# Performance work log

Measured on AMD Instinct MI355X. Metric: run time of the kernel, lower is better.

## Reference

```python
import jax, jax.numpy as jnp
import numpy as np

NUM_GROUPS = 5
EPS = 1e-5
QB = 128.0  # 2**(8-1) for b=8 activation quantization


def _binarize_weights_groupwise(W):
    """Sign-binarize W group-wise along out-feature dim, STE on backward.
    Faithful to torch: rows beyond num_groups*group_size remain zero."""
    n_out = W.shape[0]
    gs = n_out // NUM_GROUPS
    Wb = jnp.zeros_like(W)
    for g in range(NUM_GROUPS):  # small fixed loop (5 groups)
        wg = W[g * gs:(g + 1) * gs]
        z = wg - wg.mean()
        # STE: forward = sign(z), backward = identity w.r.t. z
        ste = z + jax.lax.stop_gradient(jnp.sign(z) - z)
        Wb = Wb.at[g * gs:(g + 1) * gs].set(ste)
    return Wb


def _quantize_activations_groupwise(x):
    """8-bit absmax quantization group-wise along dim 0 (batch), per torch code."""
    n = x.shape[0]
    gs = n // NUM_GROUPS
    xq = jnp.zeros_like(x)
    for g in range(NUM_GROUPS):
        ag = x[g * gs:(g + 1) * gs]
        gamma = jnp.max(jnp.abs(ag))
        xq = xq.at[g * gs:(g + 1) * gs].set(
            jnp.clip(ag * QB / (gamma + EPS), -QB + EPS, QB - EPS))
    return xq


def _bitlinear(x, W, b):
    Wb = _binarize_weights_groupwise(W)
    y = jnp.einsum('btc,oc->bto', x, Wb) + b
    return _quantize_activations_groupwise(y)


def setup_inputs() -> dict:
    key = jax.random.key(0)
    k1, k2, k3, k4, k5 = jax.random.split(key, 5)
    B, T, C = 10, 2048, 384
    H = 4 * C
    lim1 = 1.0 / np.sqrt(C)
    lim2 = 1.0 / np.sqrt(H)
    x = jax.random.normal(k1, (B, T, C), dtype=jnp.float32)
    W1 = jax.random.uniform(k2, (H, C), minval=-lim1, maxval=lim1, dtype=jnp.float32)
    b1 = jax.random.uniform(k3, (H,), minval=-lim1, maxval=lim1, dtype=jnp.float32)
    W2 = jax.random.uniform(k4, (C, H), minval=-lim2, maxval=lim2, dtype=jnp.float32)
    b2 = jax.random.uniform(k5, (C,), minval=-lim2, maxval=lim2, dtype=jnp.float32)
    return {"x": x, "W1": W1, "b1": b1, "W2": W2, "b2": b2}


def reference(x, W1, b1, W2, b2):
    h = _bitlinear(x, W1, b1)           # [B,T,4C], quantized to [-128,128]
    h = jax.nn.gelu(h, approximate=False)  # torch nn.GELU default is exact
    out = _bitlinear(h, W2, b2)         # [B,T,C]
    return out  # nn.Dropout is identity in eval/reference mode
```

## Files before the change

### kernel.cpp

```cpp
#include <hip/hip_runtime.h>
#include <cstdint>
#include <cstddef>

#define THREADS 256
#define NB 8

typedef float f32x4 __attribute__((ext_vector_type(4)));
typedef __bf16 bf16x8 __attribute__((ext_vector_type(8)));
typedef __bf16 bf16x4 __attribute__((ext_vector_type(4)));

__device__ __forceinline__ void gload_lds16(const void* g, void* l) {
    auto gp = (const __attribute__((address_space(1))) unsigned int*)(unsigned long long)(uintptr_t)g;
    auto lp = (__attribute__((address_space(3))) unsigned int*)(unsigned int)(uintptr_t)l;
    __builtin_amdgcn_global_load_lds(gp, lp, 16, 0, 0);
}

__global__ void zero_gamma(unsigned int* p) {
    if (threadIdx.x < 16) p[threadIdx.x] = 0u;
}

__global__ void group_partial_sums(const float* __restrict__ W, float* __restrict__ partials,
                                   int elems_per_group) {
    const int g = blockIdx.y, b = blockIdx.x;
    const int tid = threadIdx.x;
    const int chunk4 = elems_per_group / (4 * NB);
    const float* base = W + (size_t)g * elems_per_group + (size_t)b * chunk4 * 4;
    float s = 0.f;
    for (int i = tid; i < chunk4; i += THREADS) {
        f32x4 v = *reinterpret_cast<const f32x4*>(base + 4 * (size_t)i);
        s += (v[0] + v[1]) + (v[2] + v[3]);
    }
    __shared__ float red[THREADS];
    red[tid] = s;
    __syncthreads();
    for (int off = THREADS / 2; off > 0; off >>= 1) {
        if (tid < off) red[tid] += red[tid + off];
        __syncthreads();
    }
    if (tid == 0) partials[g * NB + b] = red[0];
}

__global__ void binarize_apply(const float* __restrict__ W, __bf16* __restrict__ Wb,
                               const float* __restrict__ partials,
                               int elems_per_group, int tail_elems) {
    const int g = blockIdx.y, b = blockIdx.x;
    const int tid = threadIdx.x;
    if (g == 5) {
        if (b != 0) return;
        __bf16* og = Wb + (size_t)5 * elems_per_group;
        for (int i = tid; i < tail_elems; i += THREADS) og[i] = (__bf16)0.f;
        return;
    }
    float total = 0.f;
#pragma unroll
    for (int j = 0; j < NB; ++j) total += partials[g * NB + j];
    const float mean = total / (float)elems_per_group;

    const int chunk4 = elems_per_group / (4 * NB);
    const size_t off0 = (size_t)g * elems_per_group + (size_t)b * chunk4 * 4;
    const float* base = W + off0;
    __bf16* ob = Wb + off0;
    for (int i = tid; i < chunk4; i += THREADS) {
        f32x4 v = *reinterpret_cast<const f32x4*>(base + 4 * (size_t)i);
        bf16x4 o;
#pragma unroll
        for (int j = 0; j < 4; ++j) {
            const float z = v[j] - mean;
            o[j] = (__bf16)((z > 0.f) ? 1.f : ((z < 0.f) ? -1.f : 0.f));
        }
        *reinterpret_cast<bf16x4*>(ob + 4 * (size_t)i) = o;
    }
}

__global__ __launch_bounds__(512, 2)
void gemm1_f32a(const float* __restrict__ A, const __bf16* __restrict__ Bw,
                const float* __restrict__ bias, __bf16* __restrict__ outp,
                unsigned int* __restrict__ gmax, int M, int N, int K,
                int GN, int nwg) {
    constexpr int BM = 256, BN = 256, BK = 64, NF = 4;
    constexpr int ABYTES = BM * BK * 2;
    constexpr int BBYTES = BN * BK * 2;
    __shared__ __attribute__((aligned(16))) char lds[2 * (ABYTES + BBYTES)];

    const int tid = threadIdx.x;
    const int wave = tid >> 6, lane = tid & 63;
    const int l15 = lane & 15, l4 = lane >> 4;
    const int wr = wave >> 2, wc = wave & 3;

    const int cpx = nwg >> 3;
    const int orig = (blockIdx.x & 7) * cpx + (blockIdx.x >> 3);
    const int bm = orig / GN, bn = orig % GN;

    const int arow = tid >> 1;
    const int ach = tid & 1;
    const float* Aptr = A + (size_t)(bm * BM + arow) * K + ach * 32;
    const __bf16* Bb = Bw + (size_t)bn * BN * K;
    const int NT = K / BK;

    f32x4 acc[8][NF];
#pragma unroll
    for (int m = 0; m < 8; ++m)
#pragma unroll
        for (int n = 0; n < NF; ++n)
            acc[m][n] = f32x4{0.f, 0.f, 0.f, 0.f};

    f32x4 areg[8];
    auto LOADA = [&](int t) {
        const float* p = Aptr + t * BK;
#pragma unroll
        for (int j = 0; j < 8; ++j)
            areg[j] = *reinterpret_cast<const f32x4*>(p + j * 4);
    };
    auto WRITEA = [&](int t) {
        char* ab = lds + (t & 1) * (ABYTES + BBYTES);
#pragma unroll
        for (int j = 0; j < 4; ++j) {
            bf16x8 w;
#pragma unroll
            for (int e = 0; e < 4; ++e) {
                w[e]     = (__bf16)areg[2 * j][e];
                w[e + 4] = (__bf16)areg[2 * j + 1][e];
            }
            const int s = ach * 4 + j;
            *reinterpret_cast<bf16x8*>(
                ab + arow * 128 + ((s ^ (arow & 7)) << 4)) = w;
        }
    };
    auto STAGEB = [&](int t) {
        char* bb = lds + (t & 1) * (ABYTES + BBYTES) + ABYTES;
#pragma unroll
        for (int j = 0; j < 4; ++j) {
            const int q = j * 8192 + tid * 16;
            const int lr = q >> 7;
            const int s = ((q >> 4) & 7) ^ (lr & 7);
            gload_lds16(Bb + (size_t)lr * K + t * BK + s * 8, bb + q);
        }
    };

    LOADA(0); STAGEB(0);
    asm volatile("s_waitcnt vmcnt(0)" ::: "memory");
    WRITEA(0);
    __syncthreads();

    for (int t = 0; t < NT; ++t) {
        if (t + 1 < NT) { LOADA(t + 1); STAGEB(t + 1); }
        const char* ab = lds + (t & 1) * (ABYTES + BBYTES);
        const char* bb = ab + ABYTES;
#pragma unroll
        for (int kk = 0; kk < 2; ++kk) {
            bf16x8 af[8], bfv[NF];
#pragma unroll
            for (int m = 0; m < 8; ++m) {
                const int r = wr * 128 + m * 16 + l15;
                const int sp = (kk * 4 + l4) ^ (r & 7);
                af[m] = *reinterpret_cast<const bf16x8*>(ab + r * 128 + sp * 16);
            }
#pragma unroll
            for (int n = 0; n < NF; ++n) {
                const int r = wc * 64 + n * 16 + l15;
                const int sp = (kk * 4 + l4) ^ (r & 7);
                bfv[n] = *reinterpret_cast<const bf16x8*>(bb + r * 128 + sp * 16);
            }
#pragma unroll
            for (int m = 0; m < 8; ++m)
#pragma unroll
                for (int n = 0; n < NF; ++n)
                    acc[m][n] = __builtin_amdgcn_mfma_f32_16x16x32_bf16(
                        bfv[n], af[m], acc[m][n], 0, 0, 0);
        }
        if (t + 1 < NT) {
            asm volatile("s_waitcnt vmcnt(0)" ::: "memory");
            WRITEA(t + 1);
        }
        __syncthreads();
    }

    const int rowb = bm * BM + wr * 128;
    const int colb = bn * BN + wc * 64;
    float lmax = 0.f;
#pragma unroll
    for (int n = 0; n < NF; ++n) {
        const f32x4 bv = *reinterpret_cast<const f32x4*>(bias + colb + n * 16 + l4 * 4);
#pragma unroll
        for (int m = 0; m < 8; ++m) {
            const int row = rowb + m * 16 + l15;
            bf16x4 o;
#pragma unroll
            for (int r = 0; r < 4; ++r) {
                const float v = acc[m][n][r] + bv[r];
                lmax = fmaxf(lmax, fabsf(v));
                o[r] = (__bf16)v;
            }
            *reinterpret_cast<bf16x4*>(
                &outp[(size_t)row * N + colb + n * 16 + l4 * 4]) = o;
        }
    }
#pragma unroll
    for (int off = 32; off > 0; off >>= 1)
        lmax = fmaxf(lmax, __shfl_down(lmax, off, 64));
    float* wredmax = (float*)lds;
    if (lane == 0) wredmax[wave] = lmax;
    __syncthreads();
    if (tid == 0) {
        float bmax = wredmax[0];
#pragma unroll
        for (int w = 1; w < 8; ++w) bmax = fmaxf(bmax, wredmax[w]);
        atomicMax(gmax + (bm * BM) / 4096, __float_as_uint(bmax));
    }
}

__global__ __launch_bounds__(512, 2)
void gemm2_bt(const __bf16* __restrict__ A, const __bf16* __restrict__ Bw,
              const float* __restrict__ bias, float* __restrict__ outp,
              unsigned int* __restrict__ gmax, int M, int N, int K,
              int GN, int nwg) {
    constexpr int BM = 256, BN_ = 128, BK = 64, NF = 2;
    constexpr int ABYTES = BM * BK * 2;
    constexpr int BBYTES = BN_ * BK * 2;
    __shared__ __attribute__((aligned(16))) char lds[2 * (ABYTES + BBYTES)];

    const int tid = threadIdx.x;
    const int wave = tid >> 6, lane = tid & 63;
    const int l15 = lane & 15, l4 = lane >> 4;
    const int wr = wave >> 2, wc = wave & 3;

    const int cpx = nwg >> 3;
    const int orig = (blockIdx.x & 7) * cpx + (blockIdx.x >> 3);
    const int bm = orig / GN, bn = orig % GN;

    const __bf16* Ab = A + (size_t)bm * BM * K;
    const __bf16* Bb = Bw + (size_t)bn * BN_ * K;
    const int NT = K / BK;

    f32x4 acc[8][NF];
#pragma unroll
    for (int m = 0; m < 8; ++m)
#pragma unroll
        for (int n = 0; n < NF; ++n)
            acc[m][n] = f32x4{0.f, 0.f, 0.f, 0.f};

    auto STAGE = [&](int t) {
        const int k0 = t * BK;
        char* ab = lds + (t & 1) * (ABYTES + BBYTES);
        char* bb = ab + ABYTES;
#pragma unroll
        for (int j = 0; j < 4; ++j) {
            const int q = j * 8192 + tid * 16;
            const int lr = q >> 7;
            const int s = ((q >> 4) & 7) ^ (lr & 7);
            gload_lds16(Ab + (size_t)lr * K + k0 + s * 8, ab + q);
        }
#pragma unroll
        for (int j = 0; j < 2; ++j) {
            const int q = j * 8192 + tid * 16;
            const int lr = q >> 7;
            const int s = ((q >> 4) & 7) ^ (lr & 7);
            gload_lds16(Bb + (size_t)lr * K + k0 + s * 8, bb + q);
        }
    };

    STAGE(0);
    asm volatile("s_waitcnt vmcnt(0)" ::: "memory");
    __syncthreads();

    for (int t = 0; t < NT; ++t) {
        if (t + 1 < NT) STAGE(t + 1);
        const char* ab = lds + (t & 1) * (ABYTES + BBYTES);
        const char* bb = ab + ABYTES;
#pragma unroll
        for (int kk = 0; kk < 2; ++kk) {
            bf16x8 af[8], bfv[NF];
#pragma unroll
            for (int m = 0; m < 8; ++m) {
                const int r = wr * 128 + m * 16 + l15;
                const int sp = (kk * 4 + l4) ^ (r & 7);
                af[m] = *reinterpret_cast<const bf16x8*>(ab + r * 128 + sp * 16);
            }
#pragma unroll
            for (int n = 0; n < NF; ++n) {
                const int r = wc * 32 + n * 16 + l15;
                const int sp = (kk * 4 + l4) ^ (r & 7);
                bfv[n] = *reinterpret_cast<const bf16x8*>(bb + r * 128 + sp * 16);
            }
#pragma unroll
            for (int m = 0; m < 8; ++m)
#pragma unroll
                for (int n = 0; n < NF; ++n)
                    acc[m][n] = __builtin_amdgcn_mfma_f32_16x16x32_bf16(
                        bfv[n], af[m], acc[m][n], 0, 0, 0);
        }
        asm volatile("s_waitcnt vmcnt(0)" ::: "memory");
        __syncthreads();
    }

    const int rowb = bm * BM + wr * 128;
    const int colb = bn * BN_ + wc * 32;
    float lmax = 0.f;
#pragma unroll
    for (int n = 0; n < NF; ++n) {
        const f32x4 bv = *reinterpret_cast<const f32x4*>(bias + colb + n * 16 + l4 * 4);
#pragma unroll
        for (int m = 0; m < 8; ++m) {
            const int row = rowb + m * 16 + l15;
            f32x4 o;
#pragma unroll
            for (int r = 0; r < 4; ++r) {
                o[r] = acc[m][n][r] + bv[r];
                lmax = fmaxf(lmax, fabsf(o[r]));
            }
            *reinterpret_cast<f32x4*>(
                &outp[(size_t)row * N + colb + n * 16 + l4 * 4]) = o;
        }
    }
#pragma unroll
    for (int off = 32; off > 0; off >>= 1)
        lmax = fmaxf(lmax, __shfl_down(lmax, off, 64));
    float* wredmax = (float*)lds;
    if (lane == 0) wredmax[wave] = lmax;
    __syncthreads();
    if (tid == 0) {
        float bmax = wredmax[0];
#pragma unroll
        for (int w = 1; w < 8; ++w) bmax = fmaxf(bmax, wredmax[w]);
        atomicMax(gmax + (bm * BM) / 4096, __float_as_uint(bmax));
    }
}

__global__ void quant_gelu(__bf16* __restrict__ y, const unsigned int* __restrict__ gbits,
                           int perg8, int n8) {
    int i = blockIdx.x * blockDim.x + threadIdx.x;
    if (i >= n8) return;
    const int g = i / perg8;
    const float gamma = __uint_as_float(gbits[g]);
    const float s = 128.0f / (gamma + 1e-5f);
    bf16x8 v = *reinterpret_cast<const bf16x8*>(y + 8 * (size_t)i);
    bf16x8 o;
#pragma unroll
    for (int j = 0; j < 8; ++j) {
        float f = (float)v[j] * s;
        f = fminf(fmaxf(f, -128.0f + 1e-5f), 128.0f - 1e-5f);
        const float ge = 0.5f * f * (1.0f + erff(f * 0.70710678118654752f));
        o[j] = (__bf16)ge;
    }
    *reinterpret_cast<bf16x8*>(y + 8 * (size_t)i) = o;
}

__global__ void final_scale(float* __restrict__ y, const unsigned int* __restrict__ gbits,
                            int perg4, int n4) {
    int i = blockIdx.x * blockDim.x + threadIdx.x;
    if (i >= n4) return;
    const int g = i / perg4;
    const float gamma = __uint_as_float(gbits[g]);
    const float s = 128.0f / (gamma + 1e-5f);
    f32x4 v = *reinterpret_cast<const f32x4*>(y + 4 * (size_t)i);
    f32x4 o;
#pragma unroll
    for (int j = 0; j < 4; ++j)
        o[j] = fminf(fmaxf(v[j] * s, -128.0f + 1e-5f), 128.0f - 1e-5f);
    *reinterpret_cast<f32x4*>(y + 4 * (size_t)i) = o;
}

extern "C" void kernel_launch(void* const* d_in, const int* in_sizes, int n_in,
                              void* d_out, int out_size, void* d_ws, size_t ws_size,
                              hipStream_t stream) {
    const float* x  = (const float*)d_in[0];
    const float* W1 = (const float*)d_in[1];
    const float* b1 = (const float*)d_in[2];
    const float* W2 = (const float*)d_in[3];
    const float* b2 = (const float*)d_in[4];
    float* out = (float*)d_out;

    const int BB = 10, TT = 2048, C = 384, H = 1536;
    const int M = BB * TT;

    const int gs1 = H / 5;
    const int gs2 = C / 5;
    const int epg1 = gs1 * C;
    const int epg2 = gs2 * H;
    const int tail1 = (H - 5 * gs1) * C;
    const int tail2 = (C - 5 * gs2) * H;

    const size_t szW1b = (size_t)H * C * 2;
    const size_t szW2b = (size_t)C * H * 2;
    const size_t szY1  = (size_t)M * H * 2;

    char* p = (char*)d_ws;
    __bf16* W1b = (__bf16*)p; p += szW1b;
    __bf16* W2b = (__bf16*)p; p += szW2b;
    __bf16* y1  = (__bf16*)p; p += szY1;
    unsigned int* gamma = (unsigned int*)p; p += 64;
    float* psums = (float*)p; p += 2 * 5 * NB * 4;
    if ((size_t)(p - (char*)d_ws) > ws_size) return;

    zero_gamma<<<1, 64, 0, stream>>>(gamma);

    group_partial_sums<<<dim3(NB, 5), THREADS, 0, stream>>>(W1, psums, epg1);
    group_partial_sums<<<dim3(NB, 5), THREADS, 0, stream>>>(W2, psums + 5 * NB, epg2);
    binarize_apply<<<dim3(NB, 6), THREADS, 0, stream>>>(W1, W1b, psums, epg1, tail1);
    binarize_apply<<<dim3(NB, 6), THREADS, 0, stream>>>(W2, W2b, psums + 5 * NB, epg2, tail2);

    gemm1_f32a<<<480, 512, 0, stream>>>(
        x, W1b, b1, y1, gamma, M, H, C, H / 256, 480);

    quant_gelu<<<(M * H / 8 + THREADS - 1) / THREADS, THREADS, 0, stream>>>(
        y1, gamma, (M / 5) * H / 8, M * H / 8);

    gemm2_bt<<<240, 512, 0, stream>>>(
        y1, W2b, b2, out, gamma + 5, M, C, H, C / 128, 240);

    final_scale<<<(M * C / 4 + THREADS - 1) / THREADS, THREADS, 0, stream>>>(
        out, gamma + 5, (M / 5) * C / 4, M * C / 4);
}
```

Before: 162.9 us.

## Fuse quantize+GELU into GEMM2 A-load and pre-convert x to bf16

The standalone quant_gelu pass over the M×H intermediate is removed. GEMM2 now loads raw bf16 GEMM1 output into registers, applies group scale, clamp and exact GELU, and writes the result to LDS. In exchange, GEMM1 takes a bf16 copy of x made by a new conversion kernel, so it can use direct global-to-LDS loads for both operands. This saves a full read-write pass of the large intermediate, but each GEMM2 tile recomputes erf for its A tile three times (once per N block) and adds an extra kernel plus an x copy.

```diff
diff --git a/kernel.cpp b/kernel.cpp
--- a/kernel.cpp
+++ b/kernel.cpp
@@ -72,14 +72,23 @@
     }
 }
 
+__global__ void cvt_f32_bf16(const float* __restrict__ in, __bf16* __restrict__ ot, int n4) {
+    int i = blockIdx.x * blockDim.x + threadIdx.x;
+    if (i >= n4) return;
+    f32x4 v = *reinterpret_cast<const f32x4*>(in + 4 * (size_t)i);
+    bf16x4 o;
+    o[0] = (__bf16)v[0]; o[1] = (__bf16)v[1]; o[2] = (__bf16)v[2]; o[3] = (__bf16)v[3];
+    *reinterpret_cast<bf16x4*>(ot + 4 * (size_t)i) = o;
+}
+
 __global__ __launch_bounds__(512, 2)
-void gemm1_f32a(const float* __restrict__ A, const __bf16* __restrict__ Bw,
-                const float* __restrict__ bias, __bf16* __restrict__ outp,
-                unsigned int* __restrict__ gmax, int M, int N, int K,
-                int GN, int nwg) {
-    constexpr int BM = 256, BN = 256, BK = 64, NF = 4;
+void gemm1_bt(const __bf16* __restrict__ A, const __bf16* __restrict__ Bw,
+              const float* __restrict__ bias, __bf16* __restrict__ outp,
+              unsigned int* __restrict__ gmax, int M, int N, int K,
+              int GN, int nwg) {
+    constexpr int BM = 256, BN_ = 256, BK = 64, NF = 4;
     constexpr int ABYTES = BM * BK * 2;
-    constexpr int BBYTES = BN * BK * 2;
+    constexpr int BBYTES = BN_ * BK * 2;
     __shared__ __attribute__((aligned(16))) char lds[2 * (ABYTES + BBYTES)];
 
     const int tid = threadIdx.x;
@@ -91,10 +100,8 @@
     const int orig = (blockIdx.x & 7) * cpx + (blockIdx.x >> 3);
     const int bm = orig / GN, bn = orig % GN;
 
-    const int arow = tid >> 1;
-    const int ach = tid & 1;
-    const float* Aptr = A + (size_t)(bm * BM + arow) * K + ach * 32;
-    const __bf16* Bb = Bw + (size_t)bn * BN * K;
+    const __bf16* Ab = A + (size_t)bm * BM * K;
+    const __bf16* Bb = Bw + (size_t)bn * BN_ * K;
     const int NT = K / BK;
 
     f32x4 acc[8][NF];
@@ -104,46 +111,32 @@
         for (int n = 0; n < NF; ++n)
             acc[m][n] = f32x4{0.f, 0.f, 0.f, 0.f};
 
-    f32x4 areg[8];
-    auto LOADA = [&](int t) {
-        const float* p = Aptr + t * BK;
-#pragma unroll
-        for (int j = 0; j < 8; ++j)
-            areg[j] = *reinterpret_cast<const f32x4*>(p + j * 4);
-    };
-    auto WRITEA = [&](int t) {
+    auto STAGE = [&](int t) {
+        const int k0 = t * BK;
         char* ab = lds + (t & 1) * (ABYTES + BBYTES);
-#pragma unroll
-        for (int j = 0; j < 4; ++j) {
-            bf16x8 w;
-#pragma unroll
-            for (int e = 0; e < 4; ++e) {
-                w[e]     = (__bf16)areg[2 * j][e];
-                w[e + 4] = (__bf16)areg[2 * j + 1][e];
-            }
-            const int s = ach * 4 + j;
-            *reinterpret_cast<bf16x8*>(
-                ab + arow * 128 + ((s ^ (arow & 7)) << 4)) = w;
-        }
-    };
-    auto STAGEB = [&](int t) {
-        char* bb = lds + (t & 1) * (ABYTES + BBYTES) + ABYTES;
+        char* bb = ab + ABYTES;
 #pragma unroll
         for (int j = 0; j < 4; ++j) {
             const int q = j * 8192 + tid * 16;
             const int lr = q >> 7;
             const int s = ((q >> 4) & 7) ^ (lr & 7);
-            gload_lds16(Bb + (size_t)lr * K + t * BK + s * 8, bb + q);
+            gload_lds16(Ab + (size_t)lr * K + k0 + s * 8, ab + q);
+        }
+#pragma unroll
+        for (int j = 0; j < 4; ++j) {
+            const int q = j * 8192 + tid * 16;
+            const int lr = q >> 7;
+            const int s = ((q >> 4) & 7) ^ (lr & 7);
+            gload_lds16(Bb + (size_t)lr * K + k0 + s * 8, bb + q);
         }
     };
 
-    LOADA(0); STAGEB(0);
+    STAGE(0);
     asm volatile("s_waitcnt vmcnt(0)" ::: "memory");
-    WRITEA(0);
     __syncthreads();
 
     for (int t = 0; t < NT; ++t) {
-        if (t + 1 < NT) { LOADA(t + 1); STAGEB(t + 1); }
+        if (t + 1 < NT) STAGE(t + 1);
         const char* ab = lds + (t & 1) * (ABYTES + BBYTES);
         const char* bb = ab + ABYTES;
 #pragma unroll
@@ -168,15 +161,12 @@
                     acc[m][n] = __builtin_amdgcn_mfma_f32_16x16x32_bf16(
                         bfv[n], af[m], acc[m][n], 0, 0, 0);
         }
-        if (t + 1 < NT) {
-            asm volatile("s_waitcnt vmcnt(0)" ::: "memory");
-            WRITEA(t + 1);
-        }
+        asm volatile("s_waitcnt vmcnt(0)" ::: "memory");
         __syncthreads();
     }
 
     const int rowb = bm * BM + wr * 128;
-    const int colb = bn * BN + wc * 64;
+    const int colb = bn * BN_ + wc * 64;
     float lmax = 0.f;
 #pragma unroll
     for (int n = 0; n < NF; ++n) {
@@ -210,10 +200,11 @@
 }
 
 __global__ __launch_bounds__(512, 2)
-void gemm2_bt(const __bf16* __restrict__ A, const __bf16* __restrict__ Bw,
-              const float* __restrict__ bias, float* __restrict__ outp,
-              unsigned int* __restrict__ gmax, int M, int N, int K,
-              int GN, int nwg) {
+void gemm2_fused(const __bf16* __restrict__ A, const __bf16* __restrict__ Bw,
+                 const float* __restrict__ bias, float* __restrict__ outp,
+                 const unsigned int* __restrict__ g1bits,
+                 unsigned int* __restrict__ gmax, int M, int N, int K,
+                 int GN, int nwg) {
     constexpr int BM = 256, BN_ = 128, BK = 64, NF = 2;
     constexpr int ABYTES = BM * BK * 2;
     constexpr int BBYTES = BN_ * BK * 2;
@@ -228,7 +219,11 @@
     const int orig = (blockIdx.x & 7) * cpx + (blockIdx.x >> 3);
     const int bm = orig / GN, bn = orig % GN;
 
-    const __bf16* Ab = A + (size_t)bm * BM * K;
+    const float s1 = 128.0f / (__uint_as_float(g1bits[bm >> 4]) + 1e-5f);
+
+    const int arow = tid >> 1;
+    const int ach = tid & 1;
+    const __bf16* Aptr = A + (size_t)(bm * BM + arow) * K + ach * 32;
     const __bf16* Bb = Bw + (size_t)bn * BN_ * K;
     const int NT = K / BK;
 
@@ -239,32 +234,47 @@
         for (int n = 0; n < NF; ++n)
             acc[m][n] = f32x4{0.f, 0.f, 0.f, 0.f};
 
-    auto STAGE = [&](int t) {
-        const int k0 = t * BK;
+    bf16x8 areg[4];
+    auto LOADA = [&](int t) {
+        const __bf16* p = Aptr + t * BK;
+#pragma unroll
+        for (int j = 0; j < 4; ++j)
+            areg[j] = *reinterpret_cast<const bf16x8*>(p + j * 8);
+    };
+    auto GELU_WRITEA = [&](int t) {
         char* ab = lds + (t & 1) * (ABYTES + BBYTES);
-        char* bb = ab + ABYTES;
 #pragma unroll
         for (int j = 0; j < 4; ++j) {
-            const int q = j * 8192 + tid * 16;
-            const int lr = q >> 7;
-            const int s = ((q >> 4) & 7) ^ (lr & 7);
-            gload_lds16(Ab + (size_t)lr * K + k0 + s * 8, ab + q);
-        }
+            bf16x8 w;
+#pragma unroll
+            for (int e = 0; e < 8; ++e) {
+                float f = (float)areg[j][e] * s1;
+                f = fminf(fmaxf(f, -128.0f + 1e-5f), 128.0f - 1e-5f);
+                w[e] = (__bf16)(0.5f * f * (1.0f + erff(f * 0.70710678118654752f)));
+            }
+            const int s = ach * 4 + j;
+            *reinterpret_cast<bf16x8*>(
+                ab + arow * 128 + ((s ^ (arow & 7)) << 4)) = w;
+        }
+    };
+    auto STAGEB = [&](int t) {
+        char* bb = lds + (t & 1) * (ABYTES + BBYTES) + ABYTES;
 #pragma unroll
         for (int j = 0; j < 2; ++j) {
             const int q = j * 8192 + tid * 16;
             const int lr = q >> 7;
             const int s = ((q >> 4) & 7) ^ (lr & 7);
-            gload_lds16(Bb + (size_t)lr * K + k0 + s * 8, bb + q);
+            gload_lds16(Bb + (size_t)lr * K + t * BK + s * 8, bb + q);
         }
     };
 
-    STAGE(0);
+    LOADA(0); STAGEB(0);
     asm volatile("s_waitcnt vmcnt(0)" ::: "memory");
+    GELU_WRITEA(0);
     __syncthreads();
 
     for (int t = 0; t < NT; ++t) {
-        if (t + 1 < NT) STAGE(t + 1);
+        if (t + 1 < NT) { LOADA(t + 1); STAGEB(t + 1); }
         const char* ab = lds + (t & 1) * (ABYTES + BBYTES);
         const char* bb = ab + ABYTES;
 #pragma unroll
@@ -290,6 +300,7 @@
                         bfv[n], af[m], acc[m][n], 0, 0, 0);
         }
         asm volatile("s_waitcnt vmcnt(0)" ::: "memory");
+        if (t + 1 < NT) GELU_WRITEA(t + 1);
         __syncthreads();
     }
 
@@ -324,25 +335,6 @@
         for (int w = 1; w < 8; ++w) bmax = fmaxf(bmax, wredmax[w]);
         atomicMax(gmax + (bm * BM) / 4096, __float_as_uint(bmax));
     }
-}
-
-__global__ void quant_gelu(__bf16* __restrict__ y, const unsigned int* __restrict__ gbits,
-                           int perg8, int n8) {
-    int i = blockIdx.x * blockDim.x + threadIdx.x;
-    if (i >= n8) return;
-    const int g = i / perg8;
-    const float gamma = __uint_as_float(gbits[g]);
-    const float s = 128.0f / (gamma + 1e-5f);
-    bf16x8 v = *reinterpret_cast<const bf16x8*>(y + 8 * (size_t)i);
-    bf16x8 o;
-#pragma unroll
-    for (int j = 0; j < 8; ++j) {
-        float f = (float)v[j] * s;
-        f = fminf(fmaxf(f, -128.0f + 1e-5f), 128.0f - 1e-5f);
-        const float ge = 0.5f * f * (1.0f + erff(f * 0.70710678118654752f));
-        o[j] = (__bf16)ge;
-    }
-    *reinterpret_cast<bf16x8*>(y + 8 * (size_t)i) = o;
 }
 
 __global__ void final_scale(float* __restrict__ y, const unsigned int* __restrict__ gbits,
@@ -382,11 +374,13 @@
 
     const size_t szW1b = (size_t)H * C * 2;
     const size_t szW2b = (size_t)C * H * 2;
+    const size_t szXb  = (size_t)M * C * 2;
     const size_t szY1  = (size_t)M * H * 2;
 
     char* p = (char*)d_ws;
     __bf16* W1b = (__bf16*)p; p += szW1b;
     __bf16* W2b = (__bf16*)p; p += szW2b;
+    __bf16* xb  = (__bf16*)p; p += szXb;
     __bf16* y1  = (__bf16*)p; p += szY1;
     unsigned int* gamma = (unsigned int*)p; p += 64;
     float* psums = (float*)p; p += 2 * 5 * NB * 4;
@@ -399,14 +393,13 @@
     binarize_apply<<<dim3(NB, 6), THREADS, 0, stream>>>(W1, W1b, psums, epg1, tail1);
     binarize_apply<<<dim3(NB, 6), THREADS, 0, stream>>>(W2, W2b, psums + 5 * NB, epg2, tail2);
 
-    gemm1_f32a<<<480, 512, 0, stream>>>(
-        x, W1b, b1, y1, gamma, M, H, C, H / 256, 480);
-
-    quant_gelu<<<(M * H / 8 + THREADS - 1) / THREADS, THREADS, 0, stream>>>(
-        y1, gamma, (M / 5) * H / 8, M * H / 8);
-
-    gemm2_bt<<<240, 512, 0, stream>>>(
-        y1, W2b, b2, out, gamma + 5, M, C, H, C / 128, 240);
+    cvt_f32_bf16<<<(M * C / 4 + THREADS - 1) / THREADS, THREADS, 0, stream>>>(x, xb, M * C / 4);
+
+    gemm1_bt<<<480, 512, 0, stream>>>(
+        xb, W1b, b1, y1, gamma, M, H, C, H / 256, 480);
+
+    gemm2_fused<<<240, 512, 0, stream>>>(
+        y1, W2b, b2, out, gamma, gamma + 5, M, C, H, C / 128, 240);
 
     final_scale<<<(M * C / 4 + THREADS - 1) / THREADS, THREADS, 0, stream>>>(
         out, gamma + 5, (M / 5) * C / 4, M * C / 4);
```

Result: slower. 215.3 us (+32.2%).
